# Optimization experiments

Measured on AMD Instinct MI355X. Metric: run time of the kernel, lower is better.

## Reference

```python
import jax, jax.numpy as jnp
import numpy as np

DIM = 1024
HEADS = 16
DIM_HEAD = 64
INNER = HEADS * DIM_HEAD
EPS = 1e-5

def layernorm(x, g, b):
    mu = jnp.mean(x, axis=-1, keepdims=True)
    var = jnp.var(x, axis=-1, keepdims=True)
    return (x - mu) * jax.lax.rsqrt(var + EPS) * g + b

def setup_inputs() -> dict:
    key = jax.random.key(0)
    ks = jax.random.split(key, 9)
    b, t, n, m = 8, 8, 576, 64
    x = jax.random.normal(ks[0], (b, t, n, DIM), dtype=jnp.float32)
    latents = jax.random.normal(ks[1], (b, t, m, DIM), dtype=jnp.float32)
    att_mask = jax.random.randint(ks[2], (b, t, n), 0, 2, dtype=jnp.int32)
    s = 1.0 / np.sqrt(DIM)
    Wq = jax.random.normal(ks[3], (DIM, INNER), dtype=jnp.float32) * s
    Wkv = jax.random.normal(ks[4], (DIM, 2 * INNER), dtype=jnp.float32) * s
    Wo = jax.random.normal(ks[5], (INNER, DIM), dtype=jnp.float32) * (1.0 / np.sqrt(INNER))
    gm = jnp.ones((DIM,), jnp.float32); bm = jnp.zeros((DIM,), jnp.float32)
    gl = jnp.ones((DIM,), jnp.float32); bl = jnp.zeros((DIM,), jnp.float32)
    return {"x": x, "latents": latents, "att_mask": att_mask,
            "gm": gm, "bm": bm, "gl": gl, "bl": bl,
            "Wq": Wq, "Wkv": Wkv, "Wo": Wo}

def reference(x, latents, att_mask, gm, bm, gl, bl, Wq, Wkv, Wo):
    b, t, n, d = x.shape
    m = latents.shape[2]
    h, dh = HEADS, DIM_HEAD
    scale = dh ** -0.5

    xn = layernorm(x, gm, bm)
    ln = layernorm(latents, gl, bl)

    q = ln @ Wq                                  # b t m inner
    kv_input = jnp.concatenate((xn, ln), axis=-2)  # b t (n+m) d
    kv = kv_input @ Wkv                          # b t (n+m) 2*inner
    k, v = jnp.split(kv, 2, axis=-1)

    # b t s (h dh) -> b h t s dh
    def split_heads(a):
        bb, tt, ss, _ = a.shape
        return a.reshape(bb, tt, ss, h, dh).transpose(0, 3, 1, 2, 4)
    q = split_heads(q) * scale
    k = split_heads(k)
    v = split_heads(v)

    sim = jnp.einsum('bhtid,bhtjd->bhtij', q, k)   # b h t m (n+m)

    # mask: concat ones for latent KV positions; broadcast over heads and query dim
    full_mask = jnp.concatenate(
        [att_mask.astype(sim.dtype), jnp.ones((b, t, m), sim.dtype)], axis=2)  # b t (n+m)
    neg = jnp.finfo(sim.dtype).min
    bias = jnp.where(full_mask > 0, 0.0, neg)      # b t (n+m)
    sim = sim + bias[:, None, :, None, :]

    attn = jax.nn.softmax(sim, axis=-1)
    out = jnp.einsum('bhtij,bhtjd->bhtid', attn, v)  # b h t m dh
    out = out.transpose(0, 2, 3, 1, 4).reshape(b, t, m, h * dh)
    return out @ Wo
```

## Files before the change

### kernel.cpp

```cpp
#include <hip/hip_runtime.h>
#include <hip/hip_bf16.h>
#include <stdint.h>

#define NCTX 576
#define MLAT 64
#define SEQ 640
#define DMODEL 1024
#define NH 16
#define INNER_ 1024
#define KV_W 2048

typedef float f32x4 __attribute__((ext_vector_type(4)));
typedef __bf16 bf16x8 __attribute__((ext_vector_type(8)));
typedef unsigned short u16;
typedef unsigned int u32;
typedef unsigned long long u64;

typedef __attribute__((address_space(1))) u32 as1_u32;
typedef __attribute__((address_space(3))) u32 as3_u32;

__device__ __forceinline__ u16 f2bf(float f) {
    u32 u = __builtin_bit_cast(u32, f);
    u32 r = (u + 0x7fffu + ((u >> 16) & 1u)) >> 16;
    return (u16)r;
}

__device__ __forceinline__ int xcd_swizzle(int orig, int nwg) {
    int q = nwg >> 3, r = nwg & 7;
    int xcd = orig & 7, loc = orig >> 3;
    return (xcd < r ? xcd * (q + 1) : r * (q + 1) + (xcd - r) * q) + loc;
}

__global__ __launch_bounds__(640) void build_idx(const int* __restrict__ mask,
                                                 int* __restrict__ sidx,
                                                 int* __restrict__ cnt,
                                                 int* __restrict__ latst) {
    int bt = blockIdx.x, tid = threadIdx.x;
    __shared__ int ps[640];
    int valid = (tid < NCTX) ? (mask[bt * NCTX + tid] > 0 ? 1 : 0) : 0;
    ps[tid] = valid;
    __syncthreads();
    for (int off = 1; off < 640; off <<= 1) {
        int v = (tid >= off) ? ps[tid - off] : 0;
        __syncthreads();
        ps[tid] += v;
        __syncthreads();
    }
    int nc = ps[NCTX - 1];
    if (valid) sidx[bt * SEQ + ps[tid] - 1] = tid;
    if (tid < MLAT) sidx[bt * SEQ + nc + tid] = NCTX + tid;
    if (tid == 0) { cnt[bt] = nc + MLAT; latst[bt] = nc; }
}

__global__ __launch_bounds__(256) void transpose_cast_all(const float* __restrict__ Wq,
                                                          const float* __restrict__ Wkv,
                                                          const float* __restrict__ Wo,
                                                          u16* __restrict__ WqT,
                                                          u16* __restrict__ WkvT,
                                                          u16* __restrict__ WoT) {
    __shared__ float tile[64][65];
    int id = blockIdx.x;
    const float* src; u16* dst; int N;
    if (id < 256)      { src = Wq;  dst = WqT;  N = 1024; }
    else if (id < 768) { src = Wkv; dst = WkvT; N = 2048; id -= 256; }
    else               { src = Wo;  dst = WoT;  N = 1024; id -= 768; }
    int nx = N >> 6;
    int n0 = (id % nx) * 64, k0 = (id / nx) * 64;
    int tid = threadIdx.x;
#pragma unroll
    for (int i = 0; i < 4; ++i) {
        int idx = i * 256 + tid;
        int kk = idx >> 4;
        int nn = (idx & 15) << 2;
        float4 v = *(const float4*)(src + (u64)(k0 + kk) * N + n0 + nn);
        tile[kk][nn] = v.x; tile[kk][nn + 1] = v.y; tile[kk][nn + 2] = v.z; tile[kk][nn + 3] = v.w;
    }
    __syncthreads();
#pragma unroll
    for (int i = 0; i < 4; ++i) {
        int idx = i * 256 + tid;
        int nn = idx >> 4;
        int kk = (idx & 15) << 2;
        ushort4 o;
        o.x = f2bf(tile[kk][nn]);     o.y = f2bf(tile[kk + 1][nn]);
        o.z = f2bf(tile[kk + 2][nn]); o.w = f2bf(tile[kk + 3][nn]);
        *(ushort4*)(dst + (u64)(n0 + nn) * 1024 + k0 + kk) = o;
    }
}

__global__ __launch_bounds__(256) void ln_cast(const float* __restrict__ x,
                                               const float* __restrict__ lat,
                                               const float* __restrict__ gm, const float* __restrict__ bm,
                                               const float* __restrict__ gl, const float* __restrict__ bl,
                                               u16* __restrict__ out,
                                               const int* __restrict__ sidx, const int* __restrict__ cnt,
                                               int bt0, int nrows) {
    int w = threadIdx.x >> 6, lane = threadIdx.x & 63;
    int nw = gridDim.x * 4;
    for (int row = blockIdx.x * 4 + w; row < nrows; row += nw) {
        int btl = row / SEQ, jl = row - btl * SEQ;
        int btg = bt0 + btl;
        if (jl >= cnt[btg]) continue;
        int sp = sidx[btg * SEQ + jl];
        const float *src, *g, *b;
        if (sp < NCTX) { src = x + ((u64)btl * NCTX + sp) * DMODEL; g = gm; b = bm; }
        else           { src = lat + ((u64)btl * MLAT + (sp - NCTX)) * DMODEL; g = gl; b = bl; }
        float4 v[4];
        float sum = 0.f, sq = 0.f;
#pragma unroll
        for (int j = 0; j < 4; ++j) {
            v[j] = *(const float4*)(src + ((j * 64 + lane) << 2));
            sum += v[j].x + v[j].y + v[j].z + v[j].w;
            sq  += v[j].x * v[j].x + v[j].y * v[j].y + v[j].z * v[j].z + v[j].w * v[j].w;
        }
#pragma unroll
        for (int off = 1; off < 64; off <<= 1) {
            sum += __shfl_xor(sum, off, 64);
            sq  += __shfl_xor(sq, off, 64);
        }
        float mu = sum * (1.0f / DMODEL);
        float var = sq * (1.0f / DMODEL) - mu * mu;
        float rstd = rsqrtf(var + 1e-5f);
        u16* orow = out + (u64)row * DMODEL;
#pragma unroll
        for (int j = 0; j < 4; ++j) {
            float4 gv = *(const float4*)(g + ((j * 64 + lane) << 2));
            float4 bv = *(const float4*)(b + ((j * 64 + lane) << 2));
            ushort4 o;
            o.x = f2bf((v[j].x - mu) * rstd * gv.x + bv.x);
            o.y = f2bf((v[j].y - mu) * rstd * gv.y + bv.y);
            o.z = f2bf((v[j].z - mu) * rstd * gv.z + bv.z);
            o.w = f2bf((v[j].w - mu) * rstd * gv.w + bv.w);
            *(ushort4*)(orow + ((j * 64 + lane) << 2)) = o;
        }
    }
}

template <int VT_SPLIT, typename OUT_T>
__global__ __launch_bounds__(256) void gemm_bf16(const u16* __restrict__ A,
                                                 const u16* __restrict__ Bt,
                                                 OUT_T* __restrict__ C, u16* __restrict__ vt,
                                                 int M, int ldc, float scale,
                                                 const int* __restrict__ latstart,
                                                 const int* __restrict__ cntp, int bt0) {
    constexpr int K = 1024;
    __shared__ u16 As[128 * 32];
    __shared__ u16 Bs[128 * 32];
    int tid = threadIdx.x;
    int lane = tid & 63;
    int w = tid >> 6;
    int wm = w >> 1, wn = w & 1;
    int nwg = gridDim.x * gridDim.y;
    int wg = xcd_swizzle(blockIdx.y * gridDim.x + blockIdx.x, nwg);
    int m0 = (wg / gridDim.x) * 128;
    int n0 = (wg % gridDim.x) * 128;

    int btile = m0 / SEQ;
    if (cntp) {
        if (m0 - btile * SEQ >= cntp[bt0 + btile]) return;
    }

    f32x4 acc[4][4] = {};

    for (int k0 = 0; k0 < K; k0 += 32) {
        __syncthreads();
#pragma unroll
        for (int i = 0; i < 2; ++i) {
            int t = i * 256 + tid;
            int r = t >> 2;
            int cg = t & 3;
            int col = (cg ^ ((r >> 1) & 3)) << 3;
            int grow = m0 + r; if (grow >= M) grow = M - 1;
            u64 row;
            if (latstart) {
                int lbt = grow >> 6;
                row = (u64)lbt * SEQ + latstart[bt0 + lbt] + (grow & 63);
            } else {
                row = (u64)grow;
            }
            const u16* ga = A + row * K + k0 + col;
            __builtin_amdgcn_global_load_lds((const as1_u32*)ga,
                (as3_u32*)(As + ((i * 256 + (w << 6)) << 3)), 16, 0, 0);
            const u16* gb = Bt + (u64)(n0 + r) * K + k0 + col;
            __builtin_amdgcn_global_load_lds((const as1_u32*)gb,
                (as3_u32*)(Bs + ((i * 256 + (w << 6)) << 3)), 16, 0, 0);
        }
        __syncthreads();
        bf16x8 a[4], b[4];
        int rl = lane & 15;
        int cgl = lane >> 4;
#pragma unroll
        for (int mi = 0; mi < 4; ++mi) {
            int r = wm * 64 + mi * 16 + rl;
            int c = (cgl ^ ((r >> 1) & 3)) << 3;
            a[mi] = *(const bf16x8*)(As + r * 32 + c);
        }
#pragma unroll
        for (int ni = 0; ni < 4; ++ni) {
            int r = wn * 64 + ni * 16 + rl;
            int c = (cgl ^ ((r >> 1) & 3)) << 3;
            b[ni] = *(const bf16x8*)(Bs + r * 32 + c);
        }
#pragma unroll
        for (int mi = 0; mi < 4; ++mi)
#pragma unroll
            for (int ni = 0; ni < 4; ++ni)
                acc[mi][ni] = __builtin_amdgcn_mfma_f32_16x16x32_bf16(a[mi], b[ni], acc[mi][ni], 0, 0, 0);
    }
    int rl = lane & 15, rg = lane >> 4;
    if (VT_SPLIT && n0 >= INNER_) {
        int s0 = m0 - btile * SEQ + wm * 64;
#pragma unroll
        for (int ni = 0; ni < 4; ++ni) {
            int vcol = (n0 - INNER_) + wn * 64 + ni * 16 + rl;
            u16* vrow = vt + ((u64)btile * INNER_ + vcol) * SEQ;
#pragma unroll
            for (int mi = 0; mi < 4; ++mi) {
                int s = s0 + mi * 16 + rg * 4;
                ushort4 o;
                o.x = f2bf(acc[mi][ni][0] * scale);
                o.y = f2bf(acc[mi][ni][1] * scale);
                o.z = f2bf(acc[mi][ni][2] * scale);
                o.w = f2bf(acc[mi][ni][3] * scale);
                *(ushort4*)(vrow + s) = o;
            }
        }
    } else {
#pragma unroll
        for (int mi = 0; mi < 4; ++mi) {
#pragma unroll
            for (int r = 0; r < 4; ++r) {
                int grow = m0 + wm * 64 + mi * 16 + rg * 4 + r;
                if (grow < M) {
#pragma unroll
                    for (int ni = 0; ni < 4; ++ni) {
                        int gcol = n0 + wn * 64 + ni * 16 + rl;
                        float val = acc[mi][ni][r] * scale;
                        if constexpr (sizeof(OUT_T) == 2)
                            C[(u64)grow * ldc + gcol] = (OUT_T)f2bf(val);
                        else
                            C[(u64)grow * ldc + gcol] = val;
                    }
                }
            }
        }
    }
}

__global__ __launch_bounds__(256) void attn_kernel(const u16* __restrict__ qb,
                                                   const u16* __restrict__ kbuf,
                                                   const u16* __restrict__ vtb,
                                                   const int* __restrict__ cnt,
                                                   u16* __restrict__ ob, int bt0) {
    int h = blockIdx.x;
    int btl = blockIdx.y;
    int tid = threadIdx.x, lane = tid & 63, w = tid >> 6;
    __shared__ u16 Ks[2][64 * 64];
    __shared__ u16 Vs[2][64 * 64];
    __shared__ u16 Ps[4][16 * 64];
    __shared__ float bias_s[2][64];
    int rl = lane & 15, cgl = lane >> 4;

    int cn = cnt[bt0 + btl];
    int nch = (cn + 63) >> 6;

    bf16x8 aq[2];
    {
        int qr = btl * MLAT + w * 16 + rl;
        const u16* qp = qb + (u64)qr * INNER_ + h * 64 + cgl * 8;
        aq[0] = *(const bf16x8*)(qp);
        aq[1] = *(const bf16x8*)(qp + 32);
    }
    f32x4 acc[4] = {};
    float mrow[4], lrow[4];
#pragma unroll
    for (int r = 0; r < 4; ++r) { mrow[r] = -1e30f; lrow[r] = 0.f; }

    const u16* kbase = kbuf + (u64)btl * SEQ * INNER_ + h * 64;
    const u16* vbase = vtb + ((u64)btl * INNER_ + h * 64) * SEQ;

    auto stage = [&](int c, int bf) {
#pragma unroll
        for (int i = 0; i < 2; ++i) {
            int t = i * 256 + tid;
            int r = t >> 3, cg = t & 7;
            int col = (cg ^ (r & 7)) << 3;
            __builtin_amdgcn_global_load_lds((const as1_u32*)(kbase + (u64)(c * 64 + r) * INNER_ + col),
                (as3_u32*)(&Ks[bf][0] + ((i * 256 + (w << 6)) << 3)), 16, 0, 0);
            __builtin_amdgcn_global_load_lds((const as1_u32*)(vbase + (u64)r * SEQ + c * 64 + col),
                (as3_u32*)(&Vs[bf][0] + ((i * 256 + (w << 6)) << 3)), 16, 0, 0);
        }
        if (tid < 64) {
            int pos = c * 64 + tid;
            bias_s[bf][tid] = (pos < cn) ? 0.f : -1e30f;
        }
    };

    stage(0, 0);
    __syncthreads();

    for (int c = 0; c < nch; ++c) {
        int bf = c & 1;
        if (c + 1 < nch) stage(c + 1, bf ^ 1);

        f32x4 sf[4];
        __builtin_amdgcn_s_setprio(1);
#pragma unroll
        for (int ni = 0; ni < 4; ++ni) {
            f32x4 z = {};
#pragma unroll
            for (int kk = 0; kk < 2; ++kk) {
                int r = ni * 16 + rl;
                int g = (kk * 4 + cgl) ^ (r & 7);
                bf16x8 bk = *(const bf16x8*)(&Ks[bf][0] + r * 64 + g * 8);
                z = __builtin_amdgcn_mfma_f32_16x16x32_bf16(aq[kk], bk, z, 0, 0, 0);
            }
            float bias = bias_s[bf][ni * 16 + rl];
            z[0] += bias; z[1] += bias; z[2] += bias; z[3] += bias;
            sf[ni] = z;
        }
        __builtin_amdgcn_s_setprio(0);
        float alpha[4];
#pragma unroll
        for (int r = 0; r < 4; ++r) {
            float m = fmaxf(fmaxf(sf[0][r], sf[1][r]), fmaxf(sf[2][r], sf[3][r]));
            m = fmaxf(m, __shfl_xor(m, 1, 64));
            m = fmaxf(m, __shfl_xor(m, 2, 64));
            m = fmaxf(m, __shfl_xor(m, 4, 64));
            m = fmaxf(m, __shfl_xor(m, 8, 64));
            float mn = fmaxf(mrow[r], m);
            alpha[r] = __expf(mrow[r] - mn);
            mrow[r] = mn;
        }
#pragma unroll
        for (int ni = 0; ni < 4; ++ni)
#pragma unroll
            for (int r = 0; r < 4; ++r)
                sf[ni][r] = __expf(sf[ni][r] - mrow[r]);
#pragma unroll
        for (int r = 0; r < 4; ++r) {
            float s = sf[0][r] + sf[1][r] + sf[2][r] + sf[3][r];
            s += __shfl_xor(s, 1, 64);
            s += __shfl_xor(s, 2, 64);
            s += __shfl_xor(s, 4, 64);
            s += __shfl_xor(s, 8, 64);
            lrow[r] = lrow[r] * alpha[r] + s;
        }
        u16* pw = Ps[w];
#pragma unroll
        for (int ni = 0; ni < 4; ++ni) {
#pragma unroll
            for (int r = 0; r < 4; ++r) {
                int qrow = cgl * 4 + r;
                int kcol = ni * 16 + rl;
                int cs = (((kcol >> 3) ^ (qrow & 7)) << 3) + (kcol & 7);
                pw[qrow * 64 + cs] = f2bf(sf[ni][r]);
            }
        }
#pragma unroll
        for (int oi = 0; oi < 4; ++oi)
#pragma unroll
            for (int r = 0; r < 4; ++r)
                acc[oi][r] *= alpha[r];
        bf16x8 ap[2];
#pragma unroll
        for (int kk = 0; kk < 2; ++kk) {
            int cc = (((kk * 4 + cgl) ^ (rl & 7)) << 3);
            ap[kk] = *(const bf16x8*)(pw + rl * 64 + cc);
        }
        __builtin_amdgcn_s_setprio(1);
#pragma unroll
        for (int oi = 0; oi < 4; ++oi) {
#pragma unroll
            for (int kk = 0; kk < 2; ++kk) {
                int r = oi * 16 + rl;
                int g = (kk * 4 + cgl) ^ (r & 7);
                bf16x8 bv = *(const bf16x8*)(&Vs[bf][0] + r * 64 + g * 8);
                acc[oi] = __builtin_amdgcn_mfma_f32_16x16x32_bf16(ap[kk], bv, acc[oi], 0, 0, 0);
            }
        }
        __builtin_amdgcn_s_setprio(0);
        __syncthreads();
    }
#pragma unroll
    for (int r = 0; r < 4; ++r) {
        float inv = 1.0f / lrow[r];
        int qrow = btl * MLAT + w * 16 + cgl * 4 + r;
        u16* op = ob + (u64)qrow * INNER_ + h * 64;
#pragma unroll
        for (int oi = 0; oi < 4; ++oi)
            op[oi * 16 + rl] = f2bf(acc[oi][r] * inv);
    }
}

extern "C" void kernel_launch(void* const* d_in, const int* in_sizes, int n_in,
                              void* d_out, int out_size, void* d_ws, size_t ws_size,
                              hipStream_t stream) {
    const float* x    = (const float*)d_in[0];
    const float* lat  = (const float*)d_in[1];
    const int*   am   = (const int*)d_in[2];
    const float* gm   = (const float*)d_in[3];
    const float* bm   = (const float*)d_in[4];
    const float* gl   = (const float*)d_in[5];
    const float* bl   = (const float*)d_in[6];
    const float* Wq   = (const float*)d_in[7];
    const float* Wkv  = (const float*)d_in[8];
    const float* Wo   = (const float*)d_in[9];
    float* out = (float*)d_out;

    int* sidx  = (int*)d_ws;
    int* cnt   = sidx + 64 * SEQ;
    int* latst = cnt + 64;
    u16* WqT   = (u16*)(latst + 64);
    u16* WkvT  = WqT + 1024 * 1024;
    u16* WoT   = WkvT + 2048 * 1024;
    u16* bufs  = WoT + 1024 * 1024;

    size_t fixed = (size_t)(64 * SEQ + 128) * 4 + (size_t)(1024 * 1024 + 2048 * 1024 + 1024 * 1024) * 2;
    size_t perbt = (size_t)(SEQ * DMODEL + SEQ * INNER_ + INNER_ * SEQ + MLAT * INNER_ + MLAT * INNER_) * 2;
    int C = 64;
    while (C > 1 && fixed + (size_t)C * perbt > ws_size) C >>= 1;

    build_idx<<<64, 640, 0, stream>>>(am, sidx, cnt, latst);
    transpose_cast_all<<<1024, 256, 0, stream>>>(Wq, Wkv, Wo, WqT, WkvT, WoT);

    for (int bt0 = 0; bt0 < 64; bt0 += C) {
        u16* xn  = bufs;
        u16* kb  = xn + (size_t)C * SEQ * DMODEL;
        u16* vtp = kb + (size_t)C * SEQ * INNER_;
        u16* qbp = vtp + (size_t)C * INNER_ * SEQ;
        u16* ao  = qbp + (size_t)C * MLAT * INNER_;

        ln_cast<<<2048, 256, 0, stream>>>(x + (u64)bt0 * NCTX * DMODEL,
                                          lat + (u64)bt0 * MLAT * DMODEL,
                                          gm, bm, gl, bl, xn, sidx, cnt, bt0, C * SEQ);
        gemm_bf16<1, u16><<<dim3(KV_W / 128, (C * SEQ) / 128), 256, 0, stream>>>(
            xn, WkvT, kb, vtp, C * SEQ, INNER_, 1.0f, nullptr, cnt, bt0);
        gemm_bf16<0, u16><<<dim3(INNER_ / 128, (C * MLAT) / 128), 256, 0, stream>>>(
            xn, WqT, qbp, nullptr, C * MLAT, INNER_, 0.125f, latst, nullptr, bt0);
        attn_kernel<<<dim3(NH, C), 256, 0, stream>>>(qbp, kb, vtp, cnt, ao, bt0);
        gemm_bf16<0, float><<<dim3(DMODEL / 128, (C * MLAT) / 128), 256, 0, stream>>>(
            ao, WoT, out + (u64)bt0 * MLAT * DMODEL, nullptr, C * MLAT, DMODEL, 1.0f, nullptr, nullptr, 0);
    }
}
```

Measured before the change: 478.0 us.

## Add 256x256 double-buffered direct-to-LDS GEMM for the KV projection

Adds a new gemm256 kernel for the large KV projection. It uses 256x256 output tiles with 512 threads, a BK=64 K-step, and a double-buffered LDS pipeline filled by global_load_lds, with XOR-swizzled layout, explicit vmcnt waits and s_setprio around the MFMA blocks. The goal is better operand reuse and overlap of global loads with MFMA work on the dominant GEMM. The old generic kernel loses its V-transpose and skip paths and now only serves the Q and output projections. The bigger tiles straddle batch-tile boundaries, so the padding-skip is coarser and some skippable work is now computed; the kernel also uses about 128KB of LDS, which limits occupancy.

After: 499.9 us. +4.6%, slower.

```diff
diff --git a/kernel.cpp b/kernel.cpp
--- a/kernel.cpp
+++ b/kernel.cpp
@@ -137,12 +137,145 @@
 }
 
 template <int VT_SPLIT, typename OUT_T>
+__global__ __launch_bounds__(512) void gemm256(const u16* __restrict__ A,
+                                               const u16* __restrict__ Bt,
+                                               OUT_T* __restrict__ C, u16* __restrict__ vt,
+                                               int M, int ldc, float scale,
+                                               const int* __restrict__ cntp, int bt0) {
+    constexpr int K = 1024;
+    constexpr int BK = 64;
+    constexpr int NT = K / BK;
+    __shared__ u16 As[2][256 * BK];
+    __shared__ u16 Bs[2][256 * BK];
+    int tid = threadIdx.x;
+    int lane = tid & 63;
+    int w = tid >> 6;
+    int wm = w >> 2, wn = w & 3;
+    int nwg = gridDim.x * gridDim.y;
+    int wg = xcd_swizzle(blockIdx.y * gridDim.x + blockIdx.x, nwg);
+    int m0 = (wg / gridDim.x) * 256;
+    int n0 = (wg % gridDim.x) * 256;
+
+    if (cntp) {
+        int btile = m0 / SEQ, off = m0 - btile * SEQ;
+        if (off + 256 <= SEQ && off >= cntp[bt0 + btile]) return;
+    }
+
+    int rl = lane & 15, cgl = lane >> 4;
+
+    auto stage = [&](int t, int buf) {
+        int k0 = t * BK;
+#pragma unroll
+        for (int i = 0; i < 4; ++i) {
+            int r = i * 64 + (tid >> 3);
+            int cg = tid & 7;
+            int col = (cg ^ (r & 7)) << 3;
+            __builtin_amdgcn_global_load_lds((const as1_u32*)(A + (u64)(m0 + r) * K + k0 + col),
+                (as3_u32*)(&As[buf][0] + ((i * 512 + (w << 6)) << 3)), 16, 0, 0);
+            __builtin_amdgcn_global_load_lds((const as1_u32*)(Bt + (u64)(n0 + r) * K + k0 + col),
+                (as3_u32*)(&Bs[buf][0] + ((i * 512 + (w << 6)) << 3)), 16, 0, 0);
+        }
+    };
+
+    f32x4 acc[8][4] = {};
+
+    stage(0, 0);
+    stage(1, 1);
+    asm volatile("s_waitcnt vmcnt(8)" ::: "memory");
+    __builtin_amdgcn_s_barrier();
+    __builtin_amdgcn_sched_barrier(0);
+
+#pragma unroll 1
+    for (int t = 0; t < NT; ++t) {
+        int buf = t & 1;
+        const u16* Ab = &As[buf][0];
+        const u16* Bb = &Bs[buf][0];
+#pragma unroll
+        for (int qd = 0; qd < 4; ++qd) {
+            const int mh = qd & 1, nh = qd >> 1;
+            bf16x8 a[2][4], b[2][2];
+#pragma unroll
+            for (int kk = 0; kk < 2; ++kk) {
+#pragma unroll
+                for (int mi = 0; mi < 4; ++mi) {
+                    int r = wm * 128 + (mh * 4 + mi) * 16 + rl;
+                    int c = kk * 4 + cgl;
+                    a[kk][mi] = *(const bf16x8*)(Ab + r * BK + ((c ^ (r & 7)) << 3));
+                }
+#pragma unroll
+                for (int ni = 0; ni < 2; ++ni) {
+                    int r = wn * 64 + (nh * 2 + ni) * 16 + rl;
+                    int c = kk * 4 + cgl;
+                    b[kk][ni] = *(const bf16x8*)(Bb + r * BK + ((c ^ (r & 7)) << 3));
+                }
+            }
+            __builtin_amdgcn_s_setprio(1);
+#pragma unroll
+            for (int kk = 0; kk < 2; ++kk)
+#pragma unroll
+                for (int mi = 0; mi < 4; ++mi)
+#pragma unroll
+                    for (int ni = 0; ni < 2; ++ni)
+                        acc[mh * 4 + mi][nh * 2 + ni] = __builtin_amdgcn_mfma_f32_16x16x32_bf16(
+                            a[kk][mi], b[kk][ni], acc[mh * 4 + mi][nh * 2 + ni], 0, 0, 0);
+            __builtin_amdgcn_s_setprio(0);
+        }
+        __builtin_amdgcn_sched_barrier(0);
+        __builtin_amdgcn_s_barrier();
+        __builtin_amdgcn_sched_barrier(0);
+        if (t + 2 < NT) {
+            stage(t + 2, buf);
+            asm volatile("s_waitcnt vmcnt(8)" ::: "memory");
+        } else {
+            asm volatile("s_waitcnt vmcnt(0)" ::: "memory");
+        }
+        __builtin_amdgcn_s_barrier();
+        __builtin_amdgcn_sched_barrier(0);
+    }
+
+    if (VT_SPLIT && n0 >= INNER_) {
+#pragma unroll
+        for (int mi = 0; mi < 8; ++mi) {
+            int grow = m0 + wm * 128 + mi * 16 + cgl * 4;
+            int bt = grow / SEQ;
+            int s = grow - bt * SEQ;
+#pragma unroll
+            for (int ni = 0; ni < 4; ++ni) {
+                int vcol = (n0 - INNER_) + wn * 64 + ni * 16 + rl;
+                ushort4 o;
+                o.x = f2bf(acc[mi][ni][0] * scale);
+                o.y = f2bf(acc[mi][ni][1] * scale);
+                o.z = f2bf(acc[mi][ni][2] * scale);
+                o.w = f2bf(acc[mi][ni][3] * scale);
+                *(ushort4*)(vt + ((u64)bt * INNER_ + vcol) * SEQ + s) = o;
+            }
+        }
+    } else {
+#pragma unroll
+        for (int mi = 0; mi < 8; ++mi) {
+#pragma unroll
+            for (int r = 0; r < 4; ++r) {
+                int grow = m0 + wm * 128 + mi * 16 + cgl * 4 + r;
+#pragma unroll
+                for (int ni = 0; ni < 4; ++ni) {
+                    int gcol = n0 + wn * 64 + ni * 16 + rl;
+                    float val = acc[mi][ni][r] * scale;
+                    if constexpr (sizeof(OUT_T) == 2)
+                        C[(u64)grow * ldc + gcol] = (OUT_T)f2bf(val);
+                    else
+                        C[(u64)grow * ldc + gcol] = val;
+                }
+            }
+        }
+    }
+}
+
+template <typename OUT_T>
 __global__ __launch_bounds__(256) void gemm_bf16(const u16* __restrict__ A,
                                                  const u16* __restrict__ Bt,
-                                                 OUT_T* __restrict__ C, u16* __restrict__ vt,
+                                                 OUT_T* __restrict__ C,
                                                  int M, int ldc, float scale,
-                                                 const int* __restrict__ latstart,
-                                                 const int* __restrict__ cntp, int bt0) {
+                                                 const int* __restrict__ latstart, int bt0) {
     constexpr int K = 1024;
     __shared__ u16 As[128 * 32];
     __shared__ u16 Bs[128 * 32];
@@ -154,11 +287,6 @@
     int wg = xcd_swizzle(blockIdx.y * gridDim.x + blockIdx.x, nwg);
     int m0 = (wg / gridDim.x) * 128;
     int n0 = (wg % gridDim.x) * 128;
-
-    int btile = m0 / SEQ;
-    if (cntp) {
-        if (m0 - btile * SEQ >= cntp[bt0 + btile]) return;
-    }
 
     f32x4 acc[4][4] = {};
 
@@ -208,39 +336,20 @@
                 acc[mi][ni] = __builtin_amdgcn_mfma_f32_16x16x32_bf16(a[mi], b[ni], acc[mi][ni], 0, 0, 0);
     }
     int rl = lane & 15, rg = lane >> 4;
-    if (VT_SPLIT && n0 >= INNER_) {
-        int s0 = m0 - btile * SEQ + wm * 64;
-#pragma unroll
-        for (int ni = 0; ni < 4; ++ni) {
-            int vcol = (n0 - INNER_) + wn * 64 + ni * 16 + rl;
-            u16* vrow = vt + ((u64)btile * INNER_ + vcol) * SEQ;
-#pragma unroll
-            for (int mi = 0; mi < 4; ++mi) {
-                int s = s0 + mi * 16 + rg * 4;
-                ushort4 o;
-                o.x = f2bf(acc[mi][ni][0] * scale);
-                o.y = f2bf(acc[mi][ni][1] * scale);
-                o.z = f2bf(acc[mi][ni][2] * scale);
-                o.w = f2bf(acc[mi][ni][3] * scale);
-                *(ushort4*)(vrow + s) = o;
-            }
-        }
-    } else {
-#pragma unroll
-        for (int mi = 0; mi < 4; ++mi) {
-#pragma unroll
-            for (int r = 0; r < 4; ++r) {
-                int grow = m0 + wm * 64 + mi * 16 + rg * 4 + r;
-                if (grow < M) {
-#pragma unroll
-                    for (int ni = 0; ni < 4; ++ni) {
-                        int gcol = n0 + wn * 64 + ni * 16 + rl;
-                        float val = acc[mi][ni][r] * scale;
-                        if constexpr (sizeof(OUT_T) == 2)
-                            C[(u64)grow * ldc + gcol] = (OUT_T)f2bf(val);
-                        else
-                            C[(u64)grow * ldc + gcol] = val;
-                    }
+#pragma unroll
+    for (int mi = 0; mi < 4; ++mi) {
+#pragma unroll
+        for (int r = 0; r < 4; ++r) {
+            int grow = m0 + wm * 64 + mi * 16 + rg * 4 + r;
+            if (grow < M) {
+#pragma unroll
+                for (int ni = 0; ni < 4; ++ni) {
+                    int gcol = n0 + wn * 64 + ni * 16 + rl;
+                    float val = acc[mi][ni][r] * scale;
+                    if constexpr (sizeof(OUT_T) == 2)
+                        C[(u64)grow * ldc + gcol] = (OUT_T)f2bf(val);
+                    else
+                        C[(u64)grow * ldc + gcol] = val;
                 }
             }
         }
@@ -434,12 +543,12 @@
         ln_cast<<<2048, 256, 0, stream>>>(x + (u64)bt0 * NCTX * DMODEL,
                                           lat + (u64)bt0 * MLAT * DMODEL,
                                           gm, bm, gl, bl, xn, sidx, cnt, bt0, C * SEQ);
-        gemm_bf16<1, u16><<<dim3(KV_W / 128, (C * SEQ) / 128), 256, 0, stream>>>(
-            xn, WkvT, kb, vtp, C * SEQ, INNER_, 1.0f, nullptr, cnt, bt0);
-        gemm_bf16<0, u16><<<dim3(INNER_ / 128, (C * MLAT) / 128), 256, 0, stream>>>(
-            xn, WqT, qbp, nullptr, C * MLAT, INNER_, 0.125f, latst, nullptr, bt0);
+        gemm256<1, u16><<<dim3(KV_W / 256, (C * SEQ) / 256), 512, 0, stream>>>(
+            xn, WkvT, kb, vtp, C * SEQ, INNER_, 1.0f, cnt, bt0);
+        gemm_bf16<u16><<<dim3(INNER_ / 128, (C * MLAT) / 128), 256, 0, stream>>>(
+            xn, WqT, qbp, C * MLAT, INNER_, 0.125f, latst, bt0);
         attn_kernel<<<dim3(NH, C), 256, 0, stream>>>(qbp, kb, vtp, cnt, ao, bt0);
-        gemm_bf16<0, float><<<dim3(DMODEL / 128, (C * MLAT) / 128), 256, 0, stream>>>(
-            ao, WoT, out + (u64)bt0 * MLAT * DMODEL, nullptr, C * MLAT, DMODEL, 1.0f, nullptr, nullptr, 0);
-    }
-}
+        gemm_bf16<float><<<dim3(DMODEL / 128, (C * MLAT) / 128), 256, 0, stream>>>(
+            ao, WoT, out + (u64)bt0 * MLAT * DMODEL, C * MLAT, DMODEL, 1.0f, nullptr, 0);
+    }
+}
```
